# Performance work log

Measured on AMD Instinct MI355X. Metric: run time of the kernel, lower is better.

## Reference

```python
import jax, jax.numpy as jnp
import numpy as np

L = 8          # number of QTT cores = log2(init_reso)
RESO = 256     # init_reso
MAX_RANK = 256
N_SAMPLES = 4096


def _qtt_ranks(L, max_rank):
    return [min(8 ** k, 8 ** (L - k), max_rank) for k in range(L + 1)]


def setup_inputs() -> dict:
    key = jax.random.key(0)
    ranks = _qtt_ranks(L, MAX_RANK)
    keys = jax.random.split(key, L + 1)
    inp = {}
    for l in range(L):
        shape = (ranks[l], 8, ranks[l + 1])
        scale = (shape[0] * shape[1]) ** -0.5  # keep chain products O(1)
        inp[f"core{l}"] = jax.random.normal(keys[l], shape, dtype=jnp.float32) * scale
    inp["coords_xyz"] = jax.random.randint(keys[L], (N_SAMPLES, 3), 0, RESO)
    return inp


def _coords_to_qtt(coords_xyz, num_cores):
    # coords_xyz: (N, 3) int. Per core l (most-significant bit first):
    # c_l = 4*bit_x + 2*bit_y + bit_z in [0, 8)  -> shape (L, N)
    x, y, z = coords_xyz[:, 0], coords_xyz[:, 1], coords_xyz[:, 2]
    shifts = jnp.arange(num_cores - 1, -1, -1)[:, None]  # (L, 1)
    bx = (x[None, :] >> shifts) & 1
    by = (y[None, :] >> shifts) & 1
    bz = (z[None, :] >> shifts) & 1
    return 4 * bx + 2 * by + bz


def _sample_tt(cores, coords):
    # cores[l]: (r_l, 8, r_{l+1}); coords: (L, N)
    # v starts as first core slice: (N, r_1)  (r_0 == 1)
    v = cores[0][0, coords[0], :]
    for l in range(1, len(cores)):
        # gathered slice: (r_l, N, r_{l+1}) -> (N, r_l, r_{l+1})
        g = jnp.transpose(cores[l][:, coords[l], :], (1, 0, 2))
        v = jnp.einsum('nr,nrs->ns', v, g)
    return v[:, 0]  # r_L == 1 -> (N,)


def reference(core0, core1, core2, core3, core4, core5, core6, core7, coords_xyz):
    cores = [core0, core1, core2, core3, core4, core5, core6, core7]
    coords = _coords_to_qtt(coords_xyz, len(cores))
    return _sample_tt(cores, coords)
```

## Files before the change

kernel.cpp:

```cpp
#include <hip/hip_runtime.h>


typedef unsigned int u32;

__device__ __forceinline__ void async_load16(const float* g, float* l) {
    __builtin_amdgcn_global_load_lds(
        (const __attribute__((address_space(1))) u32*)g,
        (__attribute__((address_space(3))) u32*)l, 16, 0, 0);
}
__device__ __forceinline__ void fma4(float4& c, float a, const float4& b) {
    c.x = fmaf(a, b.x, c.x); c.y = fmaf(a, b.y, c.y);
    c.z = fmaf(a, b.z, c.z); c.w = fmaf(a, b.w, c.w);
}
__device__ __forceinline__ int digit_of(int x, int y, int z, int sh) {
    return 4*((x>>sh)&1) + 2*((y>>sh)&1) + ((z>>sh)&1);
}

__device__ __forceinline__ void kgemm_reduce_store(
    const float* __restrict__ Cd, int rowStride,
    const float (*As)[260], float* BsF,
    float* __restrict__ outP, int rowBase, int rowStep,
    int ln, int wv)
{
    const int kbase = wv * 64;
    float4 acc[8];
#pragma unroll
    for (int r = 0; r < 8; ++r) acc[r] = make_float4(0,0,0,0);

#pragma unroll 1
    for (int s = 0; s < 16; ++s) {
        if (s < 15) {
            const int nb = (s + 1) & 1;
            const int ko = kbase + (s + 1) * 4;
#pragma unroll
            for (int j = 0; j < 4; ++j)
                async_load16(Cd + (size_t)(ko + j)*rowStride + ln*4,
                             BsF + wv*2048 + nb*1024 + j*256 + ln*4);
            asm volatile("s_waitcnt vmcnt(4)" ::: "memory");
        } else {
            asm volatile("s_waitcnt vmcnt(0)" ::: "memory");
        }
        __builtin_amdgcn_sched_barrier(0);
        const int cb = s & 1, kb = kbase + s * 4;
        const float* Bp = BsF + wv*2048 + cb*1024;
        const float4 b0v = *(const float4*)(Bp +   0 + ln*4);
        const float4 b1v = *(const float4*)(Bp + 256 + ln*4);
        const float4 b2v = *(const float4*)(Bp + 512 + ln*4);
        const float4 b3v = *(const float4*)(Bp + 768 + ln*4);
#pragma unroll
        for (int r = 0; r < 8; ++r) {
            const float4 a = *(const float4*)&As[r][kb];
            fma4(acc[r], a.x, b0v); fma4(acc[r], a.y, b1v);
            fma4(acc[r], a.z, b2v); fma4(acc[r], a.w, b3v);
        }
    }

    {
        float* my = BsF + wv * 2048;
#pragma unroll
        for (int r = 0; r < 8; ++r)
            *(float4*)(my + r*256 + ln*4) = acc[r];
    }
    __syncthreads();
#pragma unroll
    for (int i = 0; i < 2; ++i) {
        const int r = wv*2 + i;
        float4 v        = *(const float4*)(BsF +        r*256 + ln*4);
        const float4 p1 = *(const float4*)(BsF + 2048 + r*256 + ln*4);
        const float4 p2 = *(const float4*)(BsF + 4096 + r*256 + ln*4);
        const float4 p3 = *(const float4*)(BsF + 6144 + r*256 + ln*4);
        v.x += p1.x + p2.x + p3.x; v.y += p1.y + p2.y + p3.y;
        v.z += p1.z + p2.z + p3.z; v.w += p1.w + p2.w + p3.w;
        *(float4*)(outP + (size_t)(rowBase + r*rowStep)*256 + ln*4) = v;
    }
}

__global__ __launch_bounds__(256, 4) void prep_kernel(
    const float* __restrict__ C4, const float* __restrict__ C5,
    const float* __restrict__ C6, const float* __restrict__ C7,
    float* __restrict__ T, float* __restrict__ C4t)
{
    const int t = threadIdx.x;
    const int bx = blockIdx.x;

    if (bx < 64) {
        __shared__ float S6s[8][64];
        const int d5 = bx >> 3, d6 = bx & 7;
#pragma unroll
        for (int j = 0; j < 2; ++j) {
            const int idx = t + 256*j, d7 = idx >> 6, s = idx & 63;
            float acc = 0.f;
#pragma unroll
            for (int jj = 0; jj < 8; ++jj)
                acc = fmaf(C6[s*64 + d6*8 + jj], C7[jj*8 + d7], acc);
            S6s[d7][s] = acc;
        }
        __syncthreads();
        float4 creg[16];
#pragma unroll
        for (int s4 = 0; s4 < 16; ++s4)
            creg[s4] = *(const float4*)(C5 + (size_t)t*512 + d5*64 + s4*4);
#pragma unroll 1
        for (int d7 = 0; d7 < 8; ++d7) {
            float acc = 0.f;
#pragma unroll
            for (int s4 = 0; s4 < 16; ++s4) {
                const float4 a = creg[s4];
                const float4 b = *(const float4*)&S6s[d7][s4*4];
                acc = fmaf(a.x, b.x, acc); acc = fmaf(a.y, b.y, acc);
                acc = fmaf(a.z, b.z, acc); acc = fmaf(a.w, b.w, acc);
            }
            T[(size_t)((d5*8 + d6)*8 + d7)*256 + t] = acc;
        }
    } else {
        const int cb = bx - 64;
        const int d4 = cb >> 2, s5q = cb & 3;
#pragma unroll 8
        for (int j = 0; j < 64; ++j) {
            const int s5 = s5q*64 + j;
            C4t[(size_t)d4*65536 + (size_t)s5*256 + t] =
                C4[(size_t)t*2048 + d4*256 + s5];
        }
    }
}

__global__ __launch_bounds__(256, 3) void tables_kernel(
    const float* __restrict__ C0, const float* __restrict__ C1,
    const float* __restrict__ C2, const float* __restrict__ C3,
    const float* __restrict__ T, const float* __restrict__ C4t,
    float* __restrict__ P3, float* __restrict__ U)
{
    __shared__ __align__(16) struct {
        float v64[8][64]; float As[8][260]; float Bs[4][2][4][256];
    } u;
    const int t = threadIdx.x;
    const int ln = t & 63, wv = t >> 6;
    const int bx = blockIdx.x;
    float* BsF = &u.Bs[0][0][0][0];
    const int kbase = wv * 64;

    if (bx < 512) {
        const int d3 = bx & 7, d2 = (bx >> 3) & 7, d0 = bx >> 6;
        const float* Cd = C3 + d3 * 256;

#pragma unroll
        for (int j = 0; j < 4; ++j)
            async_load16(Cd + (size_t)(kbase + j)*2048 + ln*4,
                         BsF + wv*2048 + j*256 + ln*4);

#pragma unroll
        for (int j = 0; j < 2; ++j) {
            const int idx = t + 256*j, d1 = idx >> 6, c = idx & 63;
            float acc = 0.f;
#pragma unroll
            for (int r = 0; r < 8; ++r)
                acc = fmaf(C0[d0*8 + r], C1[r*512 + d1*64 + c], acc);
            u.v64[d1][c] = acc;
        }
        __syncthreads();

        {
            float4 accA0 = make_float4(0,0,0,0), accA1 = make_float4(0,0,0,0);
#pragma unroll 8
            for (int j = 0; j < 64; ++j) {
                const float4 c2 = *(const float4*)(C2 + (size_t)j*2048 + d2*256 + ln*4);
                fma4(accA0, u.v64[wv*2 + 0][j], c2);
                fma4(accA1, u.v64[wv*2 + 1][j], c2);
            }
            *(float4*)&u.As[wv*2 + 0][ln*4] = accA0;
            *(float4*)&u.As[wv*2 + 1][ln*4] = accA1;
        }
        __syncthreads();

        kgemm_reduce_store(Cd, 2048, u.As, BsF,
                           P3, d0*512 + d2*8 + d3, 64, ln, wv);
    } else {
        const int ub = bx - 512;
        const int qtile = ub & 63, d4 = ub >> 6;
        const float* Cd = C4t + (size_t)d4*65536;

#pragma unroll
        for (int j = 0; j < 4; ++j)
            async_load16(Cd + (size_t)(kbase + j)*256 + ln*4,
                         BsF + wv*2048 + j*256 + ln*4);
#pragma unroll
        for (int i = 0; i < 2; ++i) {
            const int r = wv*2 + i;
            async_load16(T + (size_t)(qtile*8 + r)*256 + ln*4, &u.As[r][ln*4]);
        }
        __syncthreads();

        kgemm_reduce_store(Cd, 256, u.As, BsF,
                           U, d4*512 + qtile*8, 1, ln, wv);
    }
}

__global__ __launch_bounds__(256) void final_kernel(
    const float* __restrict__ P3, const float* __restrict__ U,
    const int* __restrict__ coords, int n, float* __restrict__ out)
{
    const int ln = threadIdx.x & 63, wv = threadIdx.x >> 6;
    const int s = blockIdx.x * 4 + wv;
    if (s >= n) return;
    const int x = coords[3*s], y = coords[3*s+1], z = coords[3*s+2];
    const int a  = digit_of(x,y,z,7)*512 + digit_of(x,y,z,6)*64
                 + digit_of(x,y,z,5)*8  + digit_of(x,y,z,4);
    const int d4 = digit_of(x,y,z,3);
    const int q  = digit_of(x,y,z,2)*64 + digit_of(x,y,z,1)*8
                 + digit_of(x,y,z,0);
    const float4 p4 = *(const float4*)(P3 + (size_t)a*256 + ln*4);
    const float4 u4 = *(const float4*)(U + (size_t)(d4*512 + q)*256 + ln*4);
    float p = fmaf(p4.x, u4.x, fmaf(p4.y, u4.y, fmaf(p4.z, u4.z, p4.w*u4.w)));
    p += __shfl_xor(p, 1);
    p += __shfl_xor(p, 2);
    p += __shfl_xor(p, 4);
    p += __shfl_xor(p, 8);
    p += __shfl_xor(p, 16);
    p += __shfl_xor(p, 32);
    if (ln == 0) out[s] = p;
}

extern "C" void kernel_launch(void* const* d_in, const int* in_sizes, int n_in,
                              void* d_out, int out_size, void* d_ws, size_t ws_size,
                              hipStream_t stream) {
    const float* C0 = (const float*)d_in[0];
    const float* C1 = (const float*)d_in[1];
    const float* C2 = (const float*)d_in[2];
    const float* C3 = (const float*)d_in[3];
    const float* C4 = (const float*)d_in[4];
    const float* C5 = (const float*)d_in[5];
    const float* C6 = (const float*)d_in[6];
    const float* C7 = (const float*)d_in[7];
    const int* coords = (const int*)d_in[8];
    float* out = (float*)d_out;

    const int n = in_sizes[8] / 3;

    float* P3  = (float*)d_ws;
    float* U   = P3  + 4096*256;
    float* Tt  = U   + 4096*256;
    float* C4t = Tt  + 512*256;

    prep_kernel<<<96, 256, 0, stream>>>(C4, C5, C6, C7, Tt, C4t);
    tables_kernel<<<1024, 256, 0, stream>>>(C0, C1, C2, C3, Tt, C4t, P3, U);
    final_kernel<<<(n + 3) / 4, 256, 0, stream>>>(P3, U, coords, n, out);
}
```

Measured before the change: 118.7 us.

## Double rows per block in table GEMM and two samples per wave in final kernel

The table-building GEMM now computes 16 output rows per block instead of 8, halving the grid to 512 blocks so each streamed B tile (C3 or C4t slice) feeds twice as many rows. The partial-sum reduction runs in two phases through the same shared buffer. The final gather kernel also handles two samples per wave to expose more memory-level parallelism. The cost is more accumulator registers (64 floats) and fewer blocks, which may lower occupancy on a GPU with many CUs.

```diff
diff --git a/kernel.cpp b/kernel.cpp
--- a/kernel.cpp
+++ b/kernel.cpp
@@ -14,65 +14,6 @@
 }
 __device__ __forceinline__ int digit_of(int x, int y, int z, int sh) {
     return 4*((x>>sh)&1) + 2*((y>>sh)&1) + ((z>>sh)&1);
-}
-
-__device__ __forceinline__ void kgemm_reduce_store(
-    const float* __restrict__ Cd, int rowStride,
-    const float (*As)[260], float* BsF,
-    float* __restrict__ outP, int rowBase, int rowStep,
-    int ln, int wv)
-{
-    const int kbase = wv * 64;
-    float4 acc[8];
-#pragma unroll
-    for (int r = 0; r < 8; ++r) acc[r] = make_float4(0,0,0,0);
-
-#pragma unroll 1
-    for (int s = 0; s < 16; ++s) {
-        if (s < 15) {
-            const int nb = (s + 1) & 1;
-            const int ko = kbase + (s + 1) * 4;
-#pragma unroll
-            for (int j = 0; j < 4; ++j)
-                async_load16(Cd + (size_t)(ko + j)*rowStride + ln*4,
-                             BsF + wv*2048 + nb*1024 + j*256 + ln*4);
-            asm volatile("s_waitcnt vmcnt(4)" ::: "memory");
-        } else {
-            asm volatile("s_waitcnt vmcnt(0)" ::: "memory");
-        }
-        __builtin_amdgcn_sched_barrier(0);
-        const int cb = s & 1, kb = kbase + s * 4;
-        const float* Bp = BsF + wv*2048 + cb*1024;
-        const float4 b0v = *(const float4*)(Bp +   0 + ln*4);
-        const float4 b1v = *(const float4*)(Bp + 256 + ln*4);
-        const float4 b2v = *(const float4*)(Bp + 512 + ln*4);
-        const float4 b3v = *(const float4*)(Bp + 768 + ln*4);
-#pragma unroll
-        for (int r = 0; r < 8; ++r) {
-            const float4 a = *(const float4*)&As[r][kb];
-            fma4(acc[r], a.x, b0v); fma4(acc[r], a.y, b1v);
-            fma4(acc[r], a.z, b2v); fma4(acc[r], a.w, b3v);
-        }
-    }
-
-    {
-        float* my = BsF + wv * 2048;
-#pragma unroll
-        for (int r = 0; r < 8; ++r)
-            *(float4*)(my + r*256 + ln*4) = acc[r];
-    }
-    __syncthreads();
-#pragma unroll
-    for (int i = 0; i < 2; ++i) {
-        const int r = wv*2 + i;
-        float4 v        = *(const float4*)(BsF +        r*256 + ln*4);
-        const float4 p1 = *(const float4*)(BsF + 2048 + r*256 + ln*4);
-        const float4 p2 = *(const float4*)(BsF + 4096 + r*256 + ln*4);
-        const float4 p3 = *(const float4*)(BsF + 6144 + r*256 + ln*4);
-        v.x += p1.x + p2.x + p3.x; v.y += p1.y + p2.y + p3.y;
-        v.z += p1.z + p2.z + p3.z; v.w += p1.w + p2.w + p3.w;
-        *(float4*)(outP + (size_t)(rowBase + r*rowStep)*256 + ln*4) = v;
-    }
 }
 
 __global__ __launch_bounds__(256, 4) void prep_kernel(
@@ -124,6 +65,69 @@
     }
 }
 
+__device__ __forceinline__ void kgemm16(
+    const float* __restrict__ Cd, int rowStride,
+    const float (*As)[260], float* BsF,
+    float* __restrict__ outP, int rowBase, int mulLo,
+    int ln, int wv)
+{
+    const int kbase = wv * 64;
+    float4 acc[16];
+#pragma unroll
+    for (int r = 0; r < 16; ++r) acc[r] = make_float4(0,0,0,0);
+
+#pragma unroll 1
+    for (int s = 0; s < 16; ++s) {
+        if (s < 15) {
+            const int nb = (s + 1) & 1;
+            const int ko = kbase + (s + 1) * 4;
+#pragma unroll
+            for (int j = 0; j < 4; ++j)
+                async_load16(Cd + (size_t)(ko + j)*rowStride + ln*4,
+                             BsF + wv*2048 + nb*1024 + j*256 + ln*4);
+            asm volatile("s_waitcnt vmcnt(4)" ::: "memory");
+        } else {
+            asm volatile("s_waitcnt vmcnt(0)" ::: "memory");
+        }
+        __builtin_amdgcn_sched_barrier(0);
+        const int cb = s & 1, kb = kbase + s * 4;
+        const float* Bp = BsF + wv*2048 + cb*1024;
+        const float4 b0v = *(const float4*)(Bp +   0 + ln*4);
+        const float4 b1v = *(const float4*)(Bp + 256 + ln*4);
+        const float4 b2v = *(const float4*)(Bp + 512 + ln*4);
+        const float4 b3v = *(const float4*)(Bp + 768 + ln*4);
+#pragma unroll
+        for (int r = 0; r < 16; ++r) {
+            const float4 a = *(const float4*)&As[r][kb];
+            fma4(acc[r], a.x, b0v); fma4(acc[r], a.y, b1v);
+            fma4(acc[r], a.z, b2v); fma4(acc[r], a.w, b3v);
+        }
+    }
+
+#pragma unroll
+    for (int ph = 0; ph < 2; ++ph) {
+        float* my = BsF + wv * 2048;
+#pragma unroll
+        for (int r8 = 0; r8 < 8; ++r8)
+            *(float4*)(my + r8*256 + ln*4) = acc[ph*8 + r8];
+        __syncthreads();
+#pragma unroll
+        for (int i = 0; i < 2; ++i) {
+            const int rr = wv*2 + i;
+            float4 v        = *(const float4*)(BsF +        rr*256 + ln*4);
+            const float4 p1 = *(const float4*)(BsF + 2048 + rr*256 + ln*4);
+            const float4 p2 = *(const float4*)(BsF + 4096 + rr*256 + ln*4);
+            const float4 p3 = *(const float4*)(BsF + 6144 + rr*256 + ln*4);
+            v.x += p1.x + p2.x + p3.x; v.y += p1.y + p2.y + p3.y;
+            v.z += p1.z + p2.z + p3.z; v.w += p1.w + p2.w + p3.w;
+            const int r = ph*8 + rr;
+            const int row = rowBase + mulLo*(r & 7) + 8*(r >> 3);
+            *(float4*)(outP + (size_t)row*256 + ln*4) = v;
+        }
+        __syncthreads();
+    }
+}
+
 __global__ __launch_bounds__(256, 3) void tables_kernel(
     const float* __restrict__ C0, const float* __restrict__ C1,
     const float* __restrict__ C2, const float* __restrict__ C3,
@@ -131,7 +135,7 @@
     float* __restrict__ P3, float* __restrict__ U)
 {
     __shared__ __align__(16) struct {
-        float v64[8][64]; float As[8][260]; float Bs[4][2][4][256];
+        float v64[8][64]; float As[16][260]; float Bs[4][2][4][256];
     } u;
     const int t = threadIdx.x;
     const int ln = t & 63, wv = t >> 6;
@@ -139,8 +143,8 @@
     float* BsF = &u.Bs[0][0][0][0];
     const int kbase = wv * 64;
 
-    if (bx < 512) {
-        const int d3 = bx & 7, d2 = (bx >> 3) & 7, d0 = bx >> 6;
+    if (bx < 256) {
+        const int d3 = bx & 7, d2p = (bx >> 3) & 3, d0 = bx >> 5;
         const float* Cd = C3 + d3 * 256;
 
 #pragma unroll
@@ -160,23 +164,29 @@
         __syncthreads();
 
         {
-            float4 accA0 = make_float4(0,0,0,0), accA1 = make_float4(0,0,0,0);
+            const int rbase = wv * 4;
+            const int d2 = d2p*2 + (rbase >> 3);
+            float4 a0 = make_float4(0,0,0,0), a1 = make_float4(0,0,0,0);
+            float4 a2 = make_float4(0,0,0,0), a3 = make_float4(0,0,0,0);
 #pragma unroll 8
             for (int j = 0; j < 64; ++j) {
                 const float4 c2 = *(const float4*)(C2 + (size_t)j*2048 + d2*256 + ln*4);
-                fma4(accA0, u.v64[wv*2 + 0][j], c2);
-                fma4(accA1, u.v64[wv*2 + 1][j], c2);
+                fma4(a0, u.v64[(rbase+0)&7][j], c2);
+                fma4(a1, u.v64[(rbase+1)&7][j], c2);
+                fma4(a2, u.v64[(rbase+2)&7][j], c2);
+                fma4(a3, u.v64[(rbase+3)&7][j], c2);
             }
-            *(float4*)&u.As[wv*2 + 0][ln*4] = accA0;
-            *(float4*)&u.As[wv*2 + 1][ln*4] = accA1;
-        }
-        __syncthreads();
-
-        kgemm_reduce_store(Cd, 2048, u.As, BsF,
-                           P3, d0*512 + d2*8 + d3, 64, ln, wv);
+            *(float4*)&u.As[rbase+0][ln*4] = a0;
+            *(float4*)&u.As[rbase+1][ln*4] = a1;
+            *(float4*)&u.As[rbase+2][ln*4] = a2;
+            *(float4*)&u.As[rbase+3][ln*4] = a3;
+        }
+        __syncthreads();
+
+        kgemm16(Cd, 2048, u.As, BsF, P3, d0*512 + d2p*16 + d3, 64, ln, wv);
     } else {
-        const int ub = bx - 512;
-        const int qtile = ub & 63, d4 = ub >> 6;
+        const int ub = bx - 256;
+        const int qtile = ub & 31, d4 = ub >> 5;
         const float* Cd = C4t + (size_t)d4*65536;
 
 #pragma unroll
@@ -184,14 +194,13 @@
             async_load16(Cd + (size_t)(kbase + j)*256 + ln*4,
                          BsF + wv*2048 + j*256 + ln*4);
 #pragma unroll
-        for (int i = 0; i < 2; ++i) {
-            const int r = wv*2 + i;
-            async_load16(T + (size_t)(qtile*8 + r)*256 + ln*4, &u.As[r][ln*4]);
-        }
-        __syncthreads();
-
-        kgemm_reduce_store(Cd, 256, u.As, BsF,
-                           U, d4*512 + qtile*8, 1, ln, wv);
+        for (int i = 0; i < 4; ++i) {
+            const int r = wv*4 + i;
+            async_load16(T + (size_t)(qtile*16 + r)*256 + ln*4, &u.As[r][ln*4]);
+        }
+        __syncthreads();
+
+        kgemm16(Cd, 256, u.As, BsF, U, d4*512 + qtile*16, 1, ln, wv);
     }
 }
 
@@ -200,24 +209,36 @@
     const int* __restrict__ coords, int n, float* __restrict__ out)
 {
     const int ln = threadIdx.x & 63, wv = threadIdx.x >> 6;
-    const int s = blockIdx.x * 4 + wv;
-    if (s >= n) return;
-    const int x = coords[3*s], y = coords[3*s+1], z = coords[3*s+2];
-    const int a  = digit_of(x,y,z,7)*512 + digit_of(x,y,z,6)*64
-                 + digit_of(x,y,z,5)*8  + digit_of(x,y,z,4);
-    const int d4 = digit_of(x,y,z,3);
-    const int q  = digit_of(x,y,z,2)*64 + digit_of(x,y,z,1)*8
-                 + digit_of(x,y,z,0);
-    const float4 p4 = *(const float4*)(P3 + (size_t)a*256 + ln*4);
-    const float4 u4 = *(const float4*)(U + (size_t)(d4*512 + q)*256 + ln*4);
-    float p = fmaf(p4.x, u4.x, fmaf(p4.y, u4.y, fmaf(p4.z, u4.z, p4.w*u4.w)));
-    p += __shfl_xor(p, 1);
-    p += __shfl_xor(p, 2);
-    p += __shfl_xor(p, 4);
-    p += __shfl_xor(p, 8);
-    p += __shfl_xor(p, 16);
-    p += __shfl_xor(p, 32);
-    if (ln == 0) out[s] = p;
+    const int s0 = blockIdx.x * 8 + wv * 2;
+
+    float p[2] = {0.f, 0.f};
+    int valid[2];
+#pragma unroll
+    for (int i = 0; i < 2; ++i) {
+        const int s = s0 + i;
+        valid[i] = (s < n);
+        if (valid[i]) {
+            const int x = coords[3*s], y = coords[3*s+1], z = coords[3*s+2];
+            const int a  = digit_of(x,y,z,7)*512 + digit_of(x,y,z,6)*64
+                         + digit_of(x,y,z,5)*8  + digit_of(x,y,z,4);
+            const int d4 = digit_of(x,y,z,3);
+            const int q  = digit_of(x,y,z,2)*64 + digit_of(x,y,z,1)*8
+                         + digit_of(x,y,z,0);
+            const float4 p4 = *(const float4*)(P3 + (size_t)a*256 + ln*4);
+            const float4 u4 = *(const float4*)(U + (size_t)(d4*512 + q)*256 + ln*4);
+            p[i] = fmaf(p4.x, u4.x, fmaf(p4.y, u4.y,
+                   fmaf(p4.z, u4.z, p4.w * u4.w)));
+        }
+    }
+#pragma unroll
+    for (int m = 1; m <= 32; m <<= 1) {
+        p[0] += __shfl_xor(p[0], m);
+        p[1] += __shfl_xor(p[1], m);
+    }
+    if (ln == 0) {
+        if (valid[0]) out[s0]     = p[0];
+        if (valid[1]) out[s0 + 1] = p[1];
+    }
 }
 
 extern "C" void kernel_launch(void* const* d_in, const int* in_sizes, int n_in,
@@ -242,6 +263,6 @@
     float* C4t = Tt  + 512*256;
 
     prep_kernel<<<96, 256, 0, stream>>>(C4, C5, C6, C7, Tt, C4t);
-    tables_kernel<<<1024, 256, 0, stream>>>(C0, C1, C2, C3, Tt, C4t, P3, U);
-    final_kernel<<<(n + 3) / 4, 256, 0, stream>>>(P3, U, coords, n, out);
-}
+    tables_kernel<<<512, 256, 0, stream>>>(C0, C1, C2, C3, Tt, C4t, P3, U);
+    final_kernel<<<(n + 7) / 8, 256, 0, stream>>>(P3, U, coords, n, out);
+}
```

Result: faster. 113.4 us (-4.4%).
